# Optimization experiments

Measured on AMD Instinct MI355X. Metric: run time of the kernel, lower is better.

## Reference

```python
import jax, jax.numpy as jnp
import numpy as np

ALPHA = 0.2  # LeakyReLU negative slope
NEG_BIG = -9e15

def setup_inputs() -> dict:
    key = jax.random.key(0)
    k1, k2, k3, k4 = jax.random.split(key, 4)
    N, Fin, Fout = 8192, 256, 64
    h = jax.random.normal(k1, (N, Fin), dtype=jnp.float32)
    adj = jax.random.randint(k2, (N, N), 0, 2, dtype=jnp.int32)
    W = jax.random.normal(k3, (Fin, Fout), dtype=jnp.float32) * 0.1
    a = jax.random.normal(k4, (2 * Fout, 1), dtype=jnp.float32) * 0.1
    return {"h": h, "adj": adj, "W": W, "a": a}

def reference(h, adj, W, a):
    Fout = W.shape[1]
    Wh = h @ W                                # [N, Fout]
    # e_ij = leakyrelu([Wh_i ; Wh_j] . a) = leakyrelu(Wh_i.a1 + Wh_j.a2)
    a1 = a[:Fout, 0]                          # [Fout]
    a2 = a[Fout:, 0]                          # [Fout]
    s1 = Wh @ a1                              # [N]
    s2 = Wh @ a2                              # [N]
    e = jax.nn.leaky_relu(s1[:, None] + s2[None, :], negative_slope=ALPHA)  # [N, N]
    attention = jnp.where(adj > 0, e, jnp.float32(NEG_BIG))
    attention = jax.nn.softmax(attention, axis=1)
    # dropout p=0.0 (eval) -> identity
    h_prime = attention @ Wh                  # [N, Fout]
    return jax.nn.elu(h_prime)                # concat=True
```

## Files before the change

### kernel.cpp

```cpp
#include <hip/hip_runtime.h>
#include <hip/hip_bf16.h>


typedef __attribute__((ext_vector_type(8))) short bf16x8;
typedef __attribute__((ext_vector_type(16))) float f32x16;

#define LOG2E 1.4426950408889634f

__device__ __forceinline__ uint pk2o(float a, float b) {
    __hip_bfloat162 h = __float22bfloat162_rn(make_float2(a, b));
    union { __hip_bfloat162 b; uint u; } c; c.b = h; return c.u;
}
__device__ __forceinline__ ushort f2bf(float x) {
    union { __hip_bfloat16 b; ushort u; } c;
    c.b = __float2bfloat16(x);
    return c.u;
}
__device__ __forceinline__ float bf2f(ushort u) {
    union { ushort u; __hip_bfloat16 b; } c;
    c.u = u;
    return __bfloat162float(c.b);
}

__global__ __launch_bounds__(256) void k1_wh(
    const float* __restrict__ h, const float* __restrict__ W,
    const float* __restrict__ a,
    float* __restrict__ s1, float* __restrict__ s2,
    ushort* __restrict__ pw_hi, ushort* __restrict__ pw_lo)
{
    __shared__ ushort whh[16][64], whl[16][64];
    const int l = threadIdx.x & 63;
    const int w = threadIdx.x >> 6;
    const int b = blockIdx.x;
    const int row0 = b * 16 + w * 4;

    float acc[4] = {0.f, 0.f, 0.f, 0.f};
    for (int k = 0; k < 256; k += 4) {
        float w0 = W[(k + 0) * 64 + l];
        float w1 = W[(k + 1) * 64 + l];
        float w2 = W[(k + 2) * 64 + l];
        float w3 = W[(k + 3) * 64 + l];
#pragma unroll
        for (int r = 0; r < 4; ++r) {
            const float4 hv = *reinterpret_cast<const float4*>(&h[(row0 + r) * 256 + k]);
            acc[r] = fmaf(hv.x, w0, acc[r]);
            acc[r] = fmaf(hv.y, w1, acc[r]);
            acc[r] = fmaf(hv.z, w2, acc[r]);
            acc[r] = fmaf(hv.w, w3, acc[r]);
        }
    }
    const float a1 = a[l];
    const float a2 = a[64 + l];
#pragma unroll
    for (int r = 0; r < 4; ++r) {
        const int row = row0 + r;
        float x1 = acc[r] * a1;
        float x2 = acc[r] * a2;
#pragma unroll
        for (int m = 32; m >= 1; m >>= 1) {
            x1 += __shfl_xor(x1, m);
            x2 += __shfl_xor(x2, m);
        }
        if (l == 0) { s1[row] = x1; s2[row] = x2 * LOG2E; }
        const ushort hi = f2bf(acc[r]);
        const ushort lo = f2bf(acc[r] - bf2f(hi));
        whh[w * 4 + r][l] = hi;
        whl[w * 4 + r][l] = lo;
    }
    __syncthreads();
    const int ft = w & 1;
    const ushort (*src)[64] = (w < 2) ? whh : whl;
    ushort* dst = (w < 2) ? pw_hi : pw_lo;
    const int hh = l >> 5;
    union { bf16x8 v; ushort s[8]; } fr;
#pragma unroll
    for (int e = 0; e < 8; ++e)
        fr.s[e] = src[hh * 8 + e][ft * 32 + (l & 31)];
    *reinterpret_cast<bf16x8*>(&dst[(size_t)(b * 2 + ft) * 512 + l * 8]) = fr.v;
}


#define PGRP(G, AV, RS) { \
    float t1_, t2_, p0_, p1_, p2_, p3_; \
    t1_ = Ag[G] + sv.x; t2_ = fmaf(0.2f, sv.x, A5g[G]); \
    p0_ = __builtin_amdgcn_exp2f(fmaxf(t1_, t2_)); if ((AV).x <= 0) p0_ = 0.f; \
    t1_ = Ag[G] + sv.y; t2_ = fmaf(0.2f, sv.y, A5g[G]); \
    p1_ = __builtin_amdgcn_exp2f(fmaxf(t1_, t2_)); if ((AV).y <= 0) p1_ = 0.f; \
    t1_ = Ag[G] + sv.z; t2_ = fmaf(0.2f, sv.z, A5g[G]); \
    p2_ = __builtin_amdgcn_exp2f(fmaxf(t1_, t2_)); if ((AV).z <= 0) p2_ = 0.f; \
    t1_ = Ag[G] + sv.w; t2_ = fmaf(0.2f, sv.w, A5g[G]); \
    p3_ = __builtin_amdgcn_exp2f(fmaxf(t1_, t2_)); if ((AV).w <= 0) p3_ = 0.f; \
    RS += (p0_ + p1_) + (p2_ + p3_); \
    *reinterpret_cast<uint2*>(&myp[(8 * (G) + g8) * 38 + jc]) = \
        make_uint2(pk2o(p0_, p1_), pk2o(p2_, p3_)); \
}

__global__ __launch_bounds__(256, 4) void k2_attn(
    const int* __restrict__ adj,
    const float* __restrict__ s1g, const float* __restrict__ s2g,
    const ushort* __restrict__ pw_hi, const ushort* __restrict__ pw_lo,
    float* __restrict__ pacc8, float* __restrict__ pden8)
{
    __shared__ __align__(16) unsigned char smem[14336];

    const int t   = threadIdx.x;
    const int l   = t & 63;
    const int wv  = t >> 6;
    const int qi  = blockIdx.x >> 3;
    const int jh  = blockIdx.x & 7;
    const int i0  = qi * 32;
    const int row = l & 31;
    const int kh  = l >> 5;
    const int g8  = l >> 3;
    const int jc  = (l & 7) * 4;

    float* s2l  = reinterpret_cast<float*>(smem);
    ushort* myp = reinterpret_cast<ushort*>(smem + 4096) + wv * 1216;
    float (*dlds)[32] = reinterpret_cast<float(*)[32]>(smem + 13824);

    reinterpret_cast<float4*>(s2l)[t] =
        reinterpret_cast<const float4*>(s2g + jh * 1024)[t];

    float Ag[4], A5g[4];
#pragma unroll
    for (int g = 0; g < 4; ++g) {
        const float s1v = s1g[i0 + 8 * g + g8];
        const float mq  = s1v + 16.0f;
        const float m   = fmaxf(mq, 0.2f * mq);
        Ag[g]  = (s1v - m) * LOG2E;
        A5g[g] = fmaf(0.2f, s1v, -m) * LOG2E;
    }
    __syncthreads();

    const int jb  = jh * 1024 + wv * 256;
    const int js0 = jb >> 4;
    const int* ap0 = adj + (size_t)(i0 + g8) * 8192 + jb + jc;
    const int* ap1 = ap0 + (size_t)8 * 8192;
    const int* ap2 = ap0 + (size_t)16 * 8192;
    const int* ap3 = ap0 + (size_t)24 * 8192;

    f32x16 acc0 = {0.f,0.f,0.f,0.f,0.f,0.f,0.f,0.f,0.f,0.f,0.f,0.f,0.f,0.f,0.f,0.f};
    f32x16 acc1 = {0.f,0.f,0.f,0.f,0.f,0.f,0.f,0.f,0.f,0.f,0.f,0.f,0.f,0.f,0.f,0.f};
    float rs0 = 0.f, rs1 = 0.f, rs2 = 0.f, rs3 = 0.f;

    int4 c0 = *reinterpret_cast<const int4*>(ap0);
    int4 c1 = *reinterpret_cast<const int4*>(ap1);
    int4 c2 = *reinterpret_cast<const int4*>(ap2);
    int4 c3 = *reinterpret_cast<const int4*>(ap3);

#pragma unroll
    for (int ms = 0; ms < 8; ++ms) {
        const int nm = (ms < 7) ? (ms + 1) * 32 : 7 * 32;
        const int4 n0 = *reinterpret_cast<const int4*>(ap0 + nm);
        const int4 n1 = *reinterpret_cast<const int4*>(ap1 + nm);
        const int4 n2 = *reinterpret_cast<const int4*>(ap2 + nm);
        const int4 n3 = *reinterpret_cast<const int4*>(ap3 + nm);
        const float4 sv = *reinterpret_cast<const float4*>(&s2l[wv * 256 + ms * 32 + jc]);

        PGRP(0, c0, rs0)
        PGRP(1, c1, rs1)
        PGRP(2, c2, rs2)
        PGRP(3, c3, rs3)

#pragma unroll
        for (int ksx = 0; ksx < 2; ++ksx) {
            const int js = js0 + ms * 2 + ksx;
            const bf16x8 ah0 = *reinterpret_cast<const bf16x8*>(&pw_hi[(size_t)(js * 2 + 0) * 512 + l * 8]);
            const bf16x8 al0 = *reinterpret_cast<const bf16x8*>(&pw_lo[(size_t)(js * 2 + 0) * 512 + l * 8]);
            const bf16x8 ah1 = *reinterpret_cast<const bf16x8*>(&pw_hi[(size_t)(js * 2 + 1) * 512 + l * 8]);
            const bf16x8 al1 = *reinterpret_cast<const bf16x8*>(&pw_lo[(size_t)(js * 2 + 1) * 512 + l * 8]);
            union { bf16x8 v; ushort4 q[2]; } bh;
            bh.q[0] = *reinterpret_cast<const ushort4*>(&myp[row * 38 + ksx * 16 + kh * 8]);
            bh.q[1] = *reinterpret_cast<const ushort4*>(&myp[row * 38 + ksx * 16 + kh * 8 + 4]);
            acc0 = __builtin_amdgcn_mfma_f32_32x32x16_bf16(ah0, bh.v, acc0, 0, 0, 0);
            acc0 = __builtin_amdgcn_mfma_f32_32x32x16_bf16(al0, bh.v, acc0, 0, 0, 0);
            acc1 = __builtin_amdgcn_mfma_f32_32x32x16_bf16(ah1, bh.v, acc1, 0, 0, 0);
            acc1 = __builtin_amdgcn_mfma_f32_32x32x16_bf16(al1, bh.v, acc1, 0, 0, 0);
        }
        c0 = n0; c1 = n1; c2 = n2; c3 = n3;
    }

#define RED8(RS) RS += __shfl_xor(RS, 1); RS += __shfl_xor(RS, 2); RS += __shfl_xor(RS, 4);
    RED8(rs0) RED8(rs1) RED8(rs2) RED8(rs3)
    if ((l & 7) == 0) {
        dlds[wv][g8]      = rs0;
        dlds[wv][8 + g8]  = rs1;
        dlds[wv][16 + g8] = rs2;
        dlds[wv][24 + g8] = rs3;
    }
    __syncthreads();

    if (wv == 0 && l < 32)
        pden8[(size_t)jh * 8192 + i0 + l] =
            dlds[0][l] + dlds[1][l] + dlds[2][l] + dlds[3][l];

    float* sldsc = reinterpret_cast<float*>(smem);
#pragma unroll
    for (int c = 0; c < 4; ++c) {
        if (wv != 0) {
            float4* d0 = reinterpret_cast<float4*>(&sldsc[(((wv - 1) * 2 + 0) * 64 + l) * 4]);
            float4* d1 = reinterpret_cast<float4*>(&sldsc[(((wv - 1) * 2 + 1) * 64 + l) * 4]);
            *d0 = make_float4(acc0[c*4+0], acc0[c*4+1], acc0[c*4+2], acc0[c*4+3]);
            *d1 = make_float4(acc1[c*4+0], acc1[c*4+1], acc1[c*4+2], acc1[c*4+3]);
        }
        __syncthreads();
        if (wv == 0) {
#pragma unroll
            for (int s = 0; s < 3; ++s) {
                const float4 v0 = *reinterpret_cast<const float4*>(&sldsc[((s * 2 + 0) * 64 + l) * 4]);
                const float4 v1 = *reinterpret_cast<const float4*>(&sldsc[((s * 2 + 1) * 64 + l) * 4]);
                acc0[c*4+0] += v0.x; acc0[c*4+1] += v0.y; acc0[c*4+2] += v0.z; acc0[c*4+3] += v0.w;
                acc1[c*4+0] += v1.x; acc1[c*4+1] += v1.y; acc1[c*4+2] += v1.z; acc1[c*4+3] += v1.w;
            }
        }
        __syncthreads();
    }

    if (wv == 0) {
        float* pb = pacc8 + ((size_t)jh * 8192 + i0 + row) * 64;
#pragma unroll
        for (int g = 0; g < 4; ++g) {
            *reinterpret_cast<float4*>(pb + 8 * g + 4 * kh) =
                make_float4(acc0[g*4+0], acc0[g*4+1], acc0[g*4+2], acc0[g*4+3]);
            *reinterpret_cast<float4*>(pb + 32 + 8 * g + 4 * kh) =
                make_float4(acc1[g*4+0], acc1[g*4+1], acc1[g*4+2], acc1[g*4+3]);
        }
    }
}

__global__ __launch_bounds__(256) void k3_fin(
    const float* __restrict__ pacc8, const float* __restrict__ pden8,
    float* __restrict__ out)
{
    const int idx = blockIdx.x * 256 + threadIdx.x;
    const int row = idx >> 4;
    float den = 0.f;
    float4 v = make_float4(0.f, 0.f, 0.f, 0.f);
#pragma unroll
    for (int p = 0; p < 8; ++p) {
        den += pden8[p * 8192 + row];
        const float4 u = reinterpret_cast<const float4*>(pacc8 + (size_t)p * 524288)[idx];
        v.x += u.x; v.y += u.y; v.z += u.z; v.w += u.w;
    }
    const float inv = 1.0f / den;
    float4 o; float x;
    x = v.x * inv; o.x = (x > 0.f) ? x : expm1f(x);
    x = v.y * inv; o.y = (x > 0.f) ? x : expm1f(x);
    x = v.z * inv; o.z = (x > 0.f) ? x : expm1f(x);
    x = v.w * inv; o.w = (x > 0.f) ? x : expm1f(x);
    reinterpret_cast<float4*>(out)[idx] = o;
}

extern "C" void kernel_launch(void* const* d_in, const int* in_sizes, int n_in,
                              void* d_out, int out_size, void* d_ws, size_t ws_size,
                              hipStream_t stream) {
    const float* h   = (const float*)d_in[0];
    const int*   adj = (const int*)d_in[1];
    const float* W   = (const float*)d_in[2];
    const float* a   = (const float*)d_in[3];
    float* out = (float*)d_out;

    float*  s1    = (float*)d_ws;
    float*  s2    = s1 + 8192;
    ushort* pw_hi = (ushort*)(s2 + 8192);
    ushort* pw_lo = pw_hi + 512 * 1024;
    float*  pacc8 = (float*)(pw_lo + 512 * 1024);
    float*  pden8 = pacc8 + 8 * 8192 * 64;

    hipLaunchKernelGGL(k1_wh, dim3(512), dim3(256), 0, stream,
                       h, W, a, s1, s2, pw_hi, pw_lo);
    hipLaunchKernelGGL(k2_attn, dim3(2048), dim3(256), 0, stream,
                       adj, s1, s2, pw_hi, pw_lo, pacc8, pden8);
    hipLaunchKernelGGL(k3_fin, dim3(512), dim3(256), 0, stream,
                       pacc8, pden8, out);
}
```

Baseline: 101.4 us.

## Double-buffer attention probability tile and fold cross-wave reduction into one pass

```diff
diff --git a/kernel.cpp b/kernel.cpp
--- a/kernel.cpp
+++ b/kernel.cpp
@@ -80,18 +80,18 @@
 }
 
 
-#define PGRP(G, AV, RS) { \
+#define PGRP(MB, G, AV, SV, RS) { \
     float t1_, t2_, p0_, p1_, p2_, p3_; \
-    t1_ = Ag[G] + sv.x; t2_ = fmaf(0.2f, sv.x, A5g[G]); \
+    t1_ = Ag[G] + (SV).x; t2_ = fmaf(0.2f, (SV).x, A5g[G]); \
     p0_ = __builtin_amdgcn_exp2f(fmaxf(t1_, t2_)); if ((AV).x <= 0) p0_ = 0.f; \
-    t1_ = Ag[G] + sv.y; t2_ = fmaf(0.2f, sv.y, A5g[G]); \
+    t1_ = Ag[G] + (SV).y; t2_ = fmaf(0.2f, (SV).y, A5g[G]); \
     p1_ = __builtin_amdgcn_exp2f(fmaxf(t1_, t2_)); if ((AV).y <= 0) p1_ = 0.f; \
-    t1_ = Ag[G] + sv.z; t2_ = fmaf(0.2f, sv.z, A5g[G]); \
+    t1_ = Ag[G] + (SV).z; t2_ = fmaf(0.2f, (SV).z, A5g[G]); \
     p2_ = __builtin_amdgcn_exp2f(fmaxf(t1_, t2_)); if ((AV).z <= 0) p2_ = 0.f; \
-    t1_ = Ag[G] + sv.w; t2_ = fmaf(0.2f, sv.w, A5g[G]); \
+    t1_ = Ag[G] + (SV).w; t2_ = fmaf(0.2f, (SV).w, A5g[G]); \
     p3_ = __builtin_amdgcn_exp2f(fmaxf(t1_, t2_)); if ((AV).w <= 0) p3_ = 0.f; \
     RS += (p0_ + p1_) + (p2_ + p3_); \
-    *reinterpret_cast<uint2*>(&myp[(8 * (G) + g8) * 38 + jc]) = \
+    *reinterpret_cast<uint2*>(&(MB)[(8 * (G) + g8) * 38 + jc]) = \
         make_uint2(pk2o(p0_, p1_), pk2o(p2_, p3_)); \
 }
 
@@ -101,7 +101,7 @@
     const ushort* __restrict__ pw_hi, const ushort* __restrict__ pw_lo,
     float* __restrict__ pacc8, float* __restrict__ pden8)
 {
-    __shared__ __align__(16) unsigned char smem[14336];
+    __shared__ __align__(16) unsigned char smem[25088];
 
     const int t   = threadIdx.x;
     const int l   = t & 63;
@@ -114,9 +114,9 @@
     const int g8  = l >> 3;
     const int jc  = (l & 7) * 4;
 
-    float* s2l  = reinterpret_cast<float*>(smem);
-    ushort* myp = reinterpret_cast<ushort*>(smem + 4096) + wv * 1216;
-    float (*dlds)[32] = reinterpret_cast<float(*)[32]>(smem + 13824);
+    float*  s2l  = reinterpret_cast<float*>(smem);
+    ushort* mypb = reinterpret_cast<ushort*>(smem + 4096) + wv * 2432;
+    float (*dlds)[32] = reinterpret_cast<float(*)[32]>(smem + 24576);
 
     reinterpret_cast<float4*>(s2l)[t] =
         reinterpret_cast<const float4*>(s2g + jh * 1024)[t];
@@ -147,37 +147,61 @@
     int4 c1 = *reinterpret_cast<const int4*>(ap1);
     int4 c2 = *reinterpret_cast<const int4*>(ap2);
     int4 c3 = *reinterpret_cast<const int4*>(ap3);
+    int4 n0 = *reinterpret_cast<const int4*>(ap0 + 32);
+    int4 n1 = *reinterpret_cast<const int4*>(ap1 + 32);
+    int4 n2 = *reinterpret_cast<const int4*>(ap2 + 32);
+    int4 n3 = *reinterpret_cast<const int4*>(ap3 + 32);
+    {
+        const float4 sv = *reinterpret_cast<const float4*>(&s2l[wv * 256 + jc]);
+        PGRP(mypb, 0, c0, sv, rs0)
+        PGRP(mypb, 1, c1, sv, rs1)
+        PGRP(mypb, 2, c2, sv, rs2)
+        PGRP(mypb, 3, c3, sv, rs3)
+    }
 
 #pragma unroll
     for (int ms = 0; ms < 8; ++ms) {
-        const int nm = (ms < 7) ? (ms + 1) * 32 : 7 * 32;
-        const int4 n0 = *reinterpret_cast<const int4*>(ap0 + nm);
-        const int4 n1 = *reinterpret_cast<const int4*>(ap1 + nm);
-        const int4 n2 = *reinterpret_cast<const int4*>(ap2 + nm);
-        const int4 n3 = *reinterpret_cast<const int4*>(ap3 + nm);
-        const float4 sv = *reinterpret_cast<const float4*>(&s2l[wv * 256 + ms * 32 + jc]);
-
-        PGRP(0, c0, rs0)
-        PGRP(1, c1, rs1)
-        PGRP(2, c2, rs2)
-        PGRP(3, c3, rs3)
-
-#pragma unroll
-        for (int ksx = 0; ksx < 2; ++ksx) {
-            const int js = js0 + ms * 2 + ksx;
-            const bf16x8 ah0 = *reinterpret_cast<const bf16x8*>(&pw_hi[(size_t)(js * 2 + 0) * 512 + l * 8]);
-            const bf16x8 al0 = *reinterpret_cast<const bf16x8*>(&pw_lo[(size_t)(js * 2 + 0) * 512 + l * 8]);
-            const bf16x8 ah1 = *reinterpret_cast<const bf16x8*>(&pw_hi[(size_t)(js * 2 + 1) * 512 + l * 8]);
-            const bf16x8 al1 = *reinterpret_cast<const bf16x8*>(&pw_lo[(size_t)(js * 2 + 1) * 512 + l * 8]);
-            union { bf16x8 v; ushort4 q[2]; } bh;
-            bh.q[0] = *reinterpret_cast<const ushort4*>(&myp[row * 38 + ksx * 16 + kh * 8]);
-            bh.q[1] = *reinterpret_cast<const ushort4*>(&myp[row * 38 + ksx * 16 + kh * 8 + 4]);
-            acc0 = __builtin_amdgcn_mfma_f32_32x32x16_bf16(ah0, bh.v, acc0, 0, 0, 0);
-            acc0 = __builtin_amdgcn_mfma_f32_32x32x16_bf16(al0, bh.v, acc0, 0, 0, 0);
-            acc1 = __builtin_amdgcn_mfma_f32_32x32x16_bf16(ah1, bh.v, acc1, 0, 0, 0);
-            acc1 = __builtin_amdgcn_mfma_f32_32x32x16_bf16(al1, bh.v, acc1, 0, 0, 0);
-        }
-        c0 = n0; c1 = n1; c2 = n2; c3 = n3;
+        const size_t jsA = (size_t)(js0 + ms * 2);
+        const bf16x8 a0h0 = *reinterpret_cast<const bf16x8*>(&pw_hi[(jsA * 2 + 0) * 512 + l * 8]);
+        const bf16x8 a0l0 = *reinterpret_cast<const bf16x8*>(&pw_lo[(jsA * 2 + 0) * 512 + l * 8]);
+        const bf16x8 a0h1 = *reinterpret_cast<const bf16x8*>(&pw_hi[(jsA * 2 + 1) * 512 + l * 8]);
+        const bf16x8 a0l1 = *reinterpret_cast<const bf16x8*>(&pw_lo[(jsA * 2 + 1) * 512 + l * 8]);
+        const bf16x8 a1h0 = *reinterpret_cast<const bf16x8*>(&pw_hi[(jsA * 2 + 2) * 512 + l * 8]);
+        const bf16x8 a1l0 = *reinterpret_cast<const bf16x8*>(&pw_lo[(jsA * 2 + 2) * 512 + l * 8]);
+        const bf16x8 a1h1 = *reinterpret_cast<const bf16x8*>(&pw_hi[(jsA * 2 + 3) * 512 + l * 8]);
+        const bf16x8 a1l1 = *reinterpret_cast<const bf16x8*>(&pw_lo[(jsA * 2 + 3) * 512 + l * 8]);
+
+        if (ms < 7) {
+            const int4 u0 = n0, u1 = n1, u2 = n2, u3 = n3;
+            if (ms < 6) {
+                const int nm = (ms + 2) * 32;
+                n0 = *reinterpret_cast<const int4*>(ap0 + nm);
+                n1 = *reinterpret_cast<const int4*>(ap1 + nm);
+                n2 = *reinterpret_cast<const int4*>(ap2 + nm);
+                n3 = *reinterpret_cast<const int4*>(ap3 + nm);
+            }
+            const float4 sv = *reinterpret_cast<const float4*>(&s2l[wv * 256 + (ms + 1) * 32 + jc]);
+            ushort* mbW = mypb + ((ms + 1) & 1) * 1216;
+            PGRP(mbW, 0, u0, sv, rs0)
+            PGRP(mbW, 1, u1, sv, rs1)
+            PGRP(mbW, 2, u2, sv, rs2)
+            PGRP(mbW, 3, u3, sv, rs3)
+        }
+
+        const ushort* mbR = mypb + (ms & 1) * 1216;
+        union { bf16x8 v; ushort4 q[2]; } b0, b1;
+        b0.q[0] = *reinterpret_cast<const ushort4*>(&mbR[row * 38 + kh * 8]);
+        b0.q[1] = *reinterpret_cast<const ushort4*>(&mbR[row * 38 + kh * 8 + 4]);
+        b1.q[0] = *reinterpret_cast<const ushort4*>(&mbR[row * 38 + 16 + kh * 8]);
+        b1.q[1] = *reinterpret_cast<const ushort4*>(&mbR[row * 38 + 16 + kh * 8 + 4]);
+        acc0 = __builtin_amdgcn_mfma_f32_32x32x16_bf16(a0h0, b0.v, acc0, 0, 0, 0);
+        acc0 = __builtin_amdgcn_mfma_f32_32x32x16_bf16(a0l0, b0.v, acc0, 0, 0, 0);
+        acc1 = __builtin_amdgcn_mfma_f32_32x32x16_bf16(a0h1, b0.v, acc1, 0, 0, 0);
+        acc1 = __builtin_amdgcn_mfma_f32_32x32x16_bf16(a0l1, b0.v, acc1, 0, 0, 0);
+        acc0 = __builtin_amdgcn_mfma_f32_32x32x16_bf16(a1h0, b1.v, acc0, 0, 0, 0);
+        acc0 = __builtin_amdgcn_mfma_f32_32x32x16_bf16(a1l0, b1.v, acc0, 0, 0, 0);
+        acc1 = __builtin_amdgcn_mfma_f32_32x32x16_bf16(a1h1, b1.v, acc1, 0, 0, 0);
+        acc1 = __builtin_amdgcn_mfma_f32_32x32x16_bf16(a1l1, b1.v, acc1, 0, 0, 0);
     }
 
 #define RED8(RS) RS += __shfl_xor(RS, 1); RS += __shfl_xor(RS, 2); RS += __shfl_xor(RS, 4);
@@ -190,33 +214,33 @@
     }
     __syncthreads();
 
+    float* slds = reinterpret_cast<float*>(smem);
+    if (wv != 0) {
+        float4* d0 = reinterpret_cast<float4*>(&slds[(((wv - 1) * 2 + 0) * 64 + l) * 16]);
+        float4* d1 = reinterpret_cast<float4*>(&slds[(((wv - 1) * 2 + 1) * 64 + l) * 16]);
+#pragma unroll
+        for (int g = 0; g < 4; ++g) {
+            d0[g] = make_float4(acc0[g*4+0], acc0[g*4+1], acc0[g*4+2], acc0[g*4+3]);
+            d1[g] = make_float4(acc1[g*4+0], acc1[g*4+1], acc1[g*4+2], acc1[g*4+3]);
+        }
+    }
     if (wv == 0 && l < 32)
         pden8[(size_t)jh * 8192 + i0 + l] =
             dlds[0][l] + dlds[1][l] + dlds[2][l] + dlds[3][l];
-
-    float* sldsc = reinterpret_cast<float*>(smem);
-#pragma unroll
-    for (int c = 0; c < 4; ++c) {
-        if (wv != 0) {
-            float4* d0 = reinterpret_cast<float4*>(&sldsc[(((wv - 1) * 2 + 0) * 64 + l) * 4]);
-            float4* d1 = reinterpret_cast<float4*>(&sldsc[(((wv - 1) * 2 + 1) * 64 + l) * 4]);
-            *d0 = make_float4(acc0[c*4+0], acc0[c*4+1], acc0[c*4+2], acc0[c*4+3]);
-            *d1 = make_float4(acc1[c*4+0], acc1[c*4+1], acc1[c*4+2], acc1[c*4+3]);
-        }
-        __syncthreads();
-        if (wv == 0) {
-#pragma unroll
-            for (int s = 0; s < 3; ++s) {
-                const float4 v0 = *reinterpret_cast<const float4*>(&sldsc[((s * 2 + 0) * 64 + l) * 4]);
-                const float4 v1 = *reinterpret_cast<const float4*>(&sldsc[((s * 2 + 1) * 64 + l) * 4]);
-                acc0[c*4+0] += v0.x; acc0[c*4+1] += v0.y; acc0[c*4+2] += v0.z; acc0[c*4+3] += v0.w;
-                acc1[c*4+0] += v1.x; acc1[c*4+1] += v1.y; acc1[c*4+2] += v1.z; acc1[c*4+3] += v1.w;
+    __syncthreads();
+
+    if (wv == 0) {
+#pragma unroll
+        for (int s = 0; s < 3; ++s) {
+            const float4* s0 = reinterpret_cast<const float4*>(&slds[((s * 2 + 0) * 64 + l) * 16]);
+            const float4* s1p = reinterpret_cast<const float4*>(&slds[((s * 2 + 1) * 64 + l) * 16]);
+#pragma unroll
+            for (int g = 0; g < 4; ++g) {
+                const float4 v0 = s0[g], v1 = s1p[g];
+                acc0[g*4+0] += v0.x; acc0[g*4+1] += v0.y; acc0[g*4+2] += v0.z; acc0[g*4+3] += v0.w;
+                acc1[g*4+0] += v1.x; acc1[g*4+1] += v1.y; acc1[g*4+2] += v1.z; acc1[g*4+3] += v1.w;
             }
         }
-        __syncthreads();
-    }
-
-    if (wv == 0) {
         float* pb = pacc8 + ((size_t)jh * 8192 + i0 + row) * 64;
 #pragma unroll
         for (int g = 0; g < 4; ++g) {
```

Measured after the change: 109.8 us. 8.3% more time.
